# Performance work log

Measured on AMD Instinct MI355X. Metric: run time of the kernel, lower is better.

Reference implementation:

```python
import jax, jax.numpy as jnp
import numpy as np

THRESHOLD_FACTOR = 1.25


def setup_inputs() -> dict:
    key = jax.random.key(0)
    B, S, D = 2, 4096, 2
    r_embed = jax.random.normal(key, (B, S, D), dtype=jnp.float32)
    return {"r_embed": r_embed}


def reference(r_embed) -> jnp.ndarray:
    # r_embed: [B, S, 2]
    B, S, _ = r_embed.shape
    diff = r_embed[:, :, None, :] - r_embed[:, None, :, :]   # [B, S, S, 2]
    dx, dy = diff[..., 0], diff[..., 1]
    dist_sq = dx * dx + dy * dy                               # [B, S, S]
    # Safe atan2: at (0,0) (diagonal) atan2 returns 0 either way; the where
    # only guards against NaN gradients, forward value is identical.
    zero_pair = (dx == 0) & (dy == 0)
    phase_diff = jnp.arctan2(jnp.where(zero_pair, 0.0, dy),
                             jnp.where(zero_pair, 1.0, dx))
    forward_bias = 0.5 * (1.0 + jnp.cos(phase_diff))          # [B, S, S]
    mean_dist = jnp.mean(dist_sq, axis=(-1, -2), keepdims=True)
    # torch.std defaults to unbiased (ddof=1)
    std_dist = jnp.std(dist_sq, axis=(-1, -2), keepdims=True, ddof=1)
    threshold = mean_dist + THRESHOLD_FACTOR * std_dist
    causal_mask = jnp.tril(jnp.ones((S, S), dtype=bool))      # [S, S]
    valid_mask = (dist_sq <= threshold) & causal_mask[None]
    attention = valid_mask.astype(r_embed.dtype) * forward_bias
    return attention
```

## Files before the change

### kernel.cpp

```cpp
#include <hip/hip_runtime.h>
#include <math.h>

__global__ void pab_moments_kernel(const float* __restrict__ r,
                                   float* __restrict__ thr_out, int S) {
    const int b = blockIdx.x;
    const float2* emb = (const float2*)r + (size_t)b * S;

    double s[12];
#pragma unroll
    for (int k = 0; k < 12; ++k) s[k] = 0.0;

    for (int idx = threadIdx.x; idx < S; idx += blockDim.x) {
        float2 p = emb[idx];
        double x = (double)p.x, y = (double)p.y;
        double x2 = x * x, y2 = y * y;
        s[0]  += x;
        s[1]  += y;
        s[2]  += x2;
        s[3]  += y2;
        s[4]  += x2 * x;
        s[5]  += y2 * y;
        s[6]  += x2 * x2;
        s[7]  += y2 * y2;
        s[8]  += x * y;
        s[9]  += x2 * y;
        s[10] += x * y2;
        s[11] += x2 * y2;
    }

    __shared__ double red[256];
    __shared__ double tot[12];
    for (int k = 0; k < 12; ++k) {
        red[threadIdx.x] = s[k];
        __syncthreads();
        for (int off = blockDim.x >> 1; off > 0; off >>= 1) {
            if ((int)threadIdx.x < off) red[threadIdx.x] += red[threadIdx.x + off];
            __syncthreads();
        }
        if (threadIdx.x == 0) tot[k] = red[0];
        __syncthreads();
    }

    if (threadIdx.x == 0) {
        double N = (double)S;
        double M = N * N;
        double S1x = tot[0], S1y = tot[1], S2x = tot[2], S2y = tot[3];
        double S3x = tot[4], S3y = tot[5], S4x = tot[6], S4y = tot[7];
        double A11 = tot[8], A21 = tot[9], A12 = tot[10], A22 = tot[11];

        double sum_d = 2.0 * N * (S2x + S2y) - 2.0 * (S1x * S1x + S1y * S1y);
        double qx = 2.0 * N * S4x - 8.0 * S3x * S1x + 6.0 * S2x * S2x;
        double qy = 2.0 * N * S4y - 8.0 * S3y * S1y + 6.0 * S2y * S2y;
        double cross = 2.0 * N * A22 - 4.0 * A21 * S1y - 4.0 * A12 * S1x
                     + 2.0 * S2x * S2y + 4.0 * A11 * A11;
        double sum_d2 = qx + qy + 2.0 * cross;

        double mean = sum_d / M;
        double var  = (sum_d2 - sum_d * sum_d / M) / (M - 1.0);
        double stdv = sqrt(var);
        thr_out[b] = (float)(mean + 1.25 * stdv);
    }
}

__global__ __launch_bounds__(256) void pab_attn_kernel(
        const float* __restrict__ r, const float* __restrict__ thr_ws,
        float* __restrict__ out, int S) {
    const int b = blockIdx.z;
    const int i = blockIdx.y;
    const int j0 = (blockIdx.x * blockDim.x + threadIdx.x) * 4;
    if (j0 >= S) return;

    const float2* emb = (const float2*)r + (size_t)b * S;
    const float2 pi = emb[i];
    const float thr = thr_ws[b];

    float4 c0 = *(const float4*)(emb + j0);
    float4 c1 = *(const float4*)(emb + j0 + 2);
    float xs[4] = {c0.x, c0.z, c1.x, c1.z};
    float ys[4] = {c0.y, c0.w, c1.y, c1.w};

    float4 res;
    float* rp = &res.x;
#pragma unroll
    for (int k = 0; k < 4; ++k) {
        float dx = pi.x - xs[k];
        float dy = pi.y - ys[k];
        float d2 = dx * dx + dy * dy;
        float bias = (d2 > 0.0f) ? (0.5f + 0.5f * dx * rsqrtf(d2)) : 1.0f;
        bool valid = (d2 <= thr) & ((j0 + k) <= i);
        rp[k] = valid ? bias : 0.0f;
    }
    *(float4*)(out + ((size_t)(b * S + i) * S + j0)) = res;
}

extern "C" void kernel_launch(void* const* d_in, const int* in_sizes, int n_in,
                              void* d_out, int out_size, void* d_ws, size_t ws_size,
                              hipStream_t stream) {
    const float* r = (const float*)d_in[0];
    float* out = (float*)d_out;
    float* thr = (float*)d_ws;

    long in0 = in_sizes[0];
    int S = (int)((2L * (long)out_size) / in0);
    int B = (int)(in0 / (2L * S));

    pab_moments_kernel<<<dim3(B), dim3(256), 0, stream>>>(r, thr, S);

    dim3 block(256);
    dim3 grid((S + 1023) / 1024, S, B);
    pab_attn_kernel<<<grid, block, 0, stream>>>(r, thr, out, S);
}
```

Measured before the change: 149.8 us.

## Process multiple rows per block and use wave-shuffle reduction for moments

The attention kernel now has each thread handle 16 output rows, reusing its loaded column embeddings and cutting the block count by 16x. The moments kernel moves to 1024 threads with vectorized float4 loads, and replaces the 12 serial shared-memory tree reductions with wave shuffles plus a small cross-wave sum. The aim is to reduce launch/scheduling overhead and the synchronization cost of the tiny prologue kernel. Fewer blocks may reduce parallelism slightly, but the output write remains the dominant, bandwidth-bound cost.

After: 144.4 us. -3.7%, faster.

```diff
diff --git a/kernel.cpp b/kernel.cpp
--- a/kernel.cpp
+++ b/kernel.cpp
@@ -1,47 +1,59 @@
 #include <hip/hip_runtime.h>
 #include <math.h>
 
-__global__ void pab_moments_kernel(const float* __restrict__ r,
-                                   float* __restrict__ thr_out, int S) {
+__global__ __launch_bounds__(1024) void pab_moments_kernel(
+        const float* __restrict__ r, float* __restrict__ thr_out, int S) {
     const int b = blockIdx.x;
     const float2* emb = (const float2*)r + (size_t)b * S;
+    const int tid = threadIdx.x;
 
     double s[12];
 #pragma unroll
     for (int k = 0; k < 12; ++k) s[k] = 0.0;
 
-    for (int idx = threadIdx.x; idx < S; idx += blockDim.x) {
-        float2 p = emb[idx];
-        double x = (double)p.x, y = (double)p.y;
-        double x2 = x * x, y2 = y * y;
-        s[0]  += x;
-        s[1]  += y;
-        s[2]  += x2;
-        s[3]  += y2;
-        s[4]  += x2 * x;
-        s[5]  += y2 * y;
-        s[6]  += x2 * x2;
-        s[7]  += y2 * y2;
-        s[8]  += x * y;
-        s[9]  += x2 * y;
-        s[10] += x * y2;
-        s[11] += x2 * y2;
+    for (int idx0 = tid * 4; idx0 < S; idx0 += blockDim.x * 4) {
+        float4 c0 = *(const float4*)(emb + idx0);
+        float4 c1 = *(const float4*)(emb + idx0 + 2);
+        float xs[4] = {c0.x, c0.z, c1.x, c1.z};
+        float ys[4] = {c0.y, c0.w, c1.y, c1.w};
+#pragma unroll
+        for (int k = 0; k < 4; ++k) {
+            if (idx0 + k >= S) break;
+            double x = (double)xs[k], y = (double)ys[k];
+            double x2 = x * x, y2 = y * y;
+            s[0]  += x;        s[1]  += y;
+            s[2]  += x2;       s[3]  += y2;
+            s[4]  += x2 * x;   s[5]  += y2 * y;
+            s[6]  += x2 * x2;  s[7]  += y2 * y2;
+            s[8]  += x * y;    s[9]  += x2 * y;
+            s[10] += x * y2;   s[11] += x2 * y2;
+        }
     }
 
-    __shared__ double red[256];
-    __shared__ double tot[12];
-    for (int k = 0; k < 12; ++k) {
-        red[threadIdx.x] = s[k];
-        __syncthreads();
-        for (int off = blockDim.x >> 1; off > 0; off >>= 1) {
-            if ((int)threadIdx.x < off) red[threadIdx.x] += red[threadIdx.x + off];
-            __syncthreads();
-        }
-        if (threadIdx.x == 0) tot[k] = red[0];
-        __syncthreads();
+#pragma unroll
+    for (int off = 32; off > 0; off >>= 1) {
+#pragma unroll
+        for (int k = 0; k < 12; ++k)
+            s[k] += __shfl_down(s[k], off, 64);
     }
 
-    if (threadIdx.x == 0) {
+    __shared__ double part[16][12];
+    __shared__ double tot[12];
+    const int wave = tid >> 6, lane = tid & 63;
+    const int nwaves = blockDim.x >> 6;
+    if (lane == 0) {
+#pragma unroll
+        for (int k = 0; k < 12; ++k) part[wave][k] = s[k];
+    }
+    __syncthreads();
+    if (tid < 12) {
+        double t = 0.0;
+        for (int w = 0; w < nwaves; ++w) t += part[w][tid];
+        tot[tid] = t;
+    }
+    __syncthreads();
+
+    if (tid == 0) {
         double N = (double)S;
         double M = N * N;
         double S1x = tot[0], S1y = tot[1], S2x = tot[2], S2y = tot[3];
@@ -57,40 +69,48 @@
 
         double mean = sum_d / M;
         double var  = (sum_d2 - sum_d * sum_d / M) / (M - 1.0);
-        double stdv = sqrt(var);
-        thr_out[b] = (float)(mean + 1.25 * stdv);
+        thr_out[b] = (float)(mean + 1.25 * sqrt(var));
     }
 }
+
+#define PAB_ROWS 16
 
 __global__ __launch_bounds__(256) void pab_attn_kernel(
         const float* __restrict__ r, const float* __restrict__ thr_ws,
         float* __restrict__ out, int S) {
     const int b = blockIdx.z;
-    const int i = blockIdx.y;
+    const int i0 = blockIdx.y * PAB_ROWS;
     const int j0 = (blockIdx.x * blockDim.x + threadIdx.x) * 4;
     if (j0 >= S) return;
 
     const float2* emb = (const float2*)r + (size_t)b * S;
-    const float2 pi = emb[i];
     const float thr = thr_ws[b];
 
     float4 c0 = *(const float4*)(emb + j0);
     float4 c1 = *(const float4*)(emb + j0 + 2);
-    float xs[4] = {c0.x, c0.z, c1.x, c1.z};
-    float ys[4] = {c0.y, c0.w, c1.y, c1.w};
+    const float xs[4] = {c0.x, c0.z, c1.x, c1.z};
+    const float ys[4] = {c0.y, c0.w, c1.y, c1.w};
 
-    float4 res;
-    float* rp = &res.x;
+    size_t orow = ((size_t)b * S + i0) * S + j0;
 #pragma unroll
-    for (int k = 0; k < 4; ++k) {
-        float dx = pi.x - xs[k];
-        float dy = pi.y - ys[k];
-        float d2 = dx * dx + dy * dy;
-        float bias = (d2 > 0.0f) ? (0.5f + 0.5f * dx * rsqrtf(d2)) : 1.0f;
-        bool valid = (d2 <= thr) & ((j0 + k) <= i);
-        rp[k] = valid ? bias : 0.0f;
+    for (int rr = 0; rr < PAB_ROWS; ++rr) {
+        const int i = i0 + rr;
+        if (i >= S) break;
+        const float2 pi = emb[i];
+        float4 res;
+        float* rp = &res.x;
+#pragma unroll
+        for (int k = 0; k < 4; ++k) {
+            float dx = pi.x - xs[k];
+            float dy = pi.y - ys[k];
+            float d2 = fmaf(dx, dx, dy * dy);
+            float bias = (d2 > 0.0f) ? fmaf(0.5f * dx, rsqrtf(d2), 0.5f) : 1.0f;
+            bool valid = (d2 <= thr) & ((j0 + k) <= i);
+            rp[k] = valid ? bias : 0.0f;
+        }
+        *(float4*)(out + orow) = res;
+        orow += S;
     }
-    *(float4*)(out + ((size_t)(b * S + i) * S + j0)) = res;
 }
 
 extern "C" void kernel_launch(void* const* d_in, const int* in_sizes, int n_in,
@@ -104,9 +124,9 @@
     int S = (int)((2L * (long)out_size) / in0);
     int B = (int)(in0 / (2L * S));
 
-    pab_moments_kernel<<<dim3(B), dim3(256), 0, stream>>>(r, thr, S);
+    pab_moments_kernel<<<dim3(B), dim3(1024), 0, stream>>>(r, thr, S);
 
     dim3 block(256);
-    dim3 grid((S + 1023) / 1024, S, B);
+    dim3 grid((S + 1023) / 1024, (S + PAB_ROWS - 1) / PAB_ROWS, B);
     pab_attn_kernel<<<grid, block, 0, stream>>>(r, thr, out, S);
 }
```
